# Kernel optimization log

Measured on AMD Instinct MI355X. Metric: run time of the kernel, lower is better.

## Reference

```python
import jax, jax.numpy as jnp
import numpy as np

B, S, D, H, DFF = 4, 1024, 1024, 16, 4096
MAX_LEN = 1024
DK = D // H
EPS = 1e-5


def _ln(x, g, b):
    m = jnp.mean(x, axis=-1, keepdims=True)
    v = jnp.mean(jnp.square(x - m), axis=-1, keepdims=True)
    return (x - m) / jnp.sqrt(v + EPS) * g + b


def setup_inputs() -> dict:
    key = jax.random.key(0)
    ks = jax.random.split(key, 16)
    s = 0.02
    inp = {
        "x": jax.random.normal(ks[0], (B, S, D), jnp.float32),
        "wq": jax.random.normal(ks[1], (D, D), jnp.float32) * s,
        "bq": jnp.zeros((D,), jnp.float32),
        "wk": jax.random.normal(ks[2], (D, D), jnp.float32) * s,
        "bk": jnp.zeros((D,), jnp.float32),
        "wv": jax.random.normal(ks[3], (D, D), jnp.float32) * s,
        "bv": jnp.zeros((D,), jnp.float32),
        "wo": jax.random.normal(ks[4], (D, D), jnp.float32) * s,
        "bo": jnp.zeros((D,), jnp.float32),
        "rel_table": jax.random.normal(ks[5], (2 * MAX_LEN - 1, H), jnp.float32) * s,
        "ln1_g": jnp.ones((D,), jnp.float32),
        "ln1_b": jnp.zeros((D,), jnp.float32),
        "w1": jax.random.normal(ks[6], (D, DFF), jnp.float32) * s,
        "b1": jnp.zeros((DFF,), jnp.float32),
        "w2": jax.random.normal(ks[7], (DFF, D), jnp.float32) * s,
        "b2": jnp.zeros((D,), jnp.float32),
        "ln2_g": jnp.ones((D,), jnp.float32),
        "ln2_b": jnp.zeros((D,), jnp.float32),
        "mask": jnp.ones((B, 1, 1, S), jnp.int32),
    }
    return inp


def reference(x, wq, bq, wk, bk, wv, bv, wo, bo, rel_table,
              ln1_g, ln1_b, w1, b1, w2, b2, ln2_g, ln2_b, mask):
    # --- multi-head attention with relative position bias (post-LN encoder layer, eval mode) ---
    q = (x @ wq + bq).reshape(B, S, H, DK).transpose(0, 2, 1, 3)  # [B,H,S,dk]
    k = (x @ wk + bk).reshape(B, S, H, DK).transpose(0, 2, 1, 3)
    v = (x @ wv + bv).reshape(B, S, H, DK).transpose(0, 2, 1, 3)

    scores = jnp.einsum('bhqd,bhkd->bhqk', q, k) / jnp.sqrt(jnp.float32(DK))

    # relative position bias: table[(q - k + max_len - 1).clip] -> [1,H,S,S]
    coords = jnp.arange(S)[:, None] - jnp.arange(S)[None, :] + (MAX_LEN - 1)
    coords = jnp.clip(coords, 0, 2 * MAX_LEN - 2)
    bias = rel_table[coords]              # [S,S,H]
    scores = scores + bias.transpose(2, 0, 1)[None]

    scores = jnp.where(mask == 0, jnp.float32(-1e9), scores)
    attn = jax.nn.softmax(scores, axis=-1)
    ctx = jnp.einsum('bhqk,bhkd->bhqd', attn, v)
    ctx = ctx.transpose(0, 2, 1, 3).reshape(B, S, D)
    attn_out = ctx @ wo + bo

    x1 = _ln(x + attn_out, ln1_g, ln1_b)

    ff = jax.nn.relu(x1 @ w1 + b1) @ w2 + b2
    return _ln(x1 + ff, ln2_g, ln2_b)
```

## Files before the change

kernel.cpp:

```cpp
#include <hip/hip_runtime.h>
#include <hip/hip_bf16.h>

typedef __hip_bfloat16 bf16;
typedef __attribute__((ext_vector_type(8))) short short8;
typedef __attribute__((ext_vector_type(4))) float f32x4;

#define LOG2E 1.4426950408889634f

typedef const __attribute__((address_space(1))) void* gptr_t;
typedef __attribute__((address_space(3))) void* sptr_t;

__device__ __forceinline__ void async16(void* lds, const void* g) {
  __builtin_amdgcn_global_load_lds((gptr_t)g, (sptr_t)lds, 16, 0, 0);
}

__device__ __forceinline__ float bf2f(unsigned short u) {
  union { unsigned int i; float f; } c; c.i = ((unsigned int)u) << 16; return c.f;
}


__global__ __launch_bounds__(256) void prep_all(
    const float* __restrict__ x, const float* __restrict__ bq,
    const float* __restrict__ bk, const float* __restrict__ bv,
    const float* __restrict__ wq, const float* __restrict__ wk,
    const float* __restrict__ wv, const float* __restrict__ wo,
    const float* __restrict__ w1, const float* __restrict__ w2,
    bf16* __restrict__ xb, float* __restrict__ bqkv,
    bf16* __restrict__ dqkv, bf16* __restrict__ dwo,
    bf16* __restrict__ dw1, bf16* __restrict__ dw2) {
  const int bid = blockIdx.x;
  if (bid < 4096) {
    int i = (bid * 256 + threadIdx.x) * 4;
    float4 v = *(const float4*)(x + i);
    bf16 h4[4] = {__float2bfloat16(v.x), __float2bfloat16(v.y),
                  __float2bfloat16(v.z), __float2bfloat16(v.w)};
    *(uint2*)((unsigned short*)xb + i) = *(uint2*)h4;
    return;
  }
  if (bid == 16384) {
#pragma unroll
    for (int j = 0; j < 12; ++j) {
      int i = j * 256 + threadIdx.x;
      bqkv[i] = (i < 1024) ? bq[i] : (i < 2048 ? bk[i - 1024] : bv[i - 2048]);
    }
    return;
  }
  __shared__ float tl[32][33];
  const int tid = bid - 4096;
  const float* s;
  bf16* d;
  int NN, KK, n0, k0;
  if (tid < 4096) {
    int m = tid >> 10, tile = tid & 1023;
    s = m == 0 ? wq : m == 1 ? wk : m == 2 ? wv : wo;
    d = m < 3 ? dqkv + (size_t)m * 1024 * 1024 : dwo;
    NN = 1024; KK = 1024;
    n0 = (tile & 31) * 32; k0 = (tile >> 5) * 32;
  } else if (tid < 8192) {
    int tile = tid - 4096;
    s = w1; d = dw1; NN = 4096; KK = 1024;
    n0 = (tile & 127) * 32; k0 = (tile >> 7) * 32;
  } else {
    int tile = tid - 8192;
    s = w2; d = dw2; NN = 1024; KK = 4096;
    n0 = (tile & 31) * 32; k0 = (tile >> 5) * 32;
  }
  const int tx = threadIdx.x & 31, ty = threadIdx.x >> 5;
#pragma unroll
  for (int j = 0; j < 4; ++j)
    tl[ty + j * 8][tx] = s[(size_t)(k0 + ty + j * 8) * NN + n0 + tx];
  __syncthreads();
#pragma unroll
  for (int j = 0; j < 4; ++j)
    d[(size_t)(n0 + ty + j * 8) * KK + k0 + tx] =
        __float2bfloat16(tl[tx][ty + j * 8]);
}


template <int RELU, int VT>
__global__ __launch_bounds__(256, 4) void gemm_bt(
    const bf16* __restrict__ A, const bf16* __restrict__ Bt,
    const float* __restrict__ bias, bf16* __restrict__ C,
    bf16* __restrict__ vt, int M, int N, int K) {
  __shared__ bf16 As[2][128 * 32];
  __shared__ bf16 Bs[2][128 * 32];
  const int t = threadIdx.x;
  const int w = t >> 6, l = t & 63;
  const int m0 = blockIdx.x * 128, n0 = blockIdx.y * 128;
  const int wr = (w >> 1) * 64, wc = (w & 1) * 64;
  const int srow = l >> 2, schunk = l & 3;
  const int lm = l & 15, lq = l >> 4;

  f32x4 acc[4][4];
#pragma unroll
  for (int i = 0; i < 4; ++i)
#pragma unroll
    for (int j = 0; j < 4; ++j) acc[i][j] = (f32x4){0.f, 0.f, 0.f, 0.f};

  auto stage = [&](int k0, int d) {
#pragma unroll
    for (int p = 0; p < 2; ++p) {
      int rbase = p * 64 + w * 16;
      int row = rbase + srow;
      int gc = schunk ^ ((row >> 1) & 3);
      async16(&As[d][rbase * 32], A + (size_t)(m0 + row) * K + k0 + gc * 8);
      async16(&Bs[d][rbase * 32], Bt + (size_t)(n0 + row) * K + k0 + gc * 8);
    }
  };

  stage(0, 0);
  const int niter = K >> 5;
  for (int it = 0; it < niter; ++it) {
    const int d = it & 1;
    __syncthreads();
    short8 af[4], bfr[4];
#pragma unroll
    for (int mi = 0; mi < 4; ++mi) {
      int rowa = wr + mi * 16 + lm;
      af[mi] = *(const short8*)&As[d][rowa * 32 + ((lq ^ ((rowa >> 1) & 3)) << 3)];
      int rowb = wc + mi * 16 + lm;
      bfr[mi] = *(const short8*)&Bs[d][rowb * 32 + ((lq ^ ((rowb >> 1) & 3)) << 3)];
    }
    if (it + 1 < niter) stage((it + 1) << 5, d ^ 1);
#pragma unroll
    for (int mi = 0; mi < 4; ++mi)
#pragma unroll
      for (int ni = 0; ni < 4; ++ni)
        acc[mi][ni] = __builtin_amdgcn_mfma_f32_16x16x32_bf16(
            af[mi], bfr[ni], acc[mi][ni], 0, 0, 0);
  }

#pragma unroll
  for (int mi = 0; mi < 4; ++mi)
#pragma unroll
    for (int ni = 0; ni < 4; ++ni) {
      int col = n0 + wc + ni * 16 + lm;
      int row0 = m0 + wr + mi * 16 + lq * 4;
      float bv = bias[col];
      float v[4];
#pragma unroll
      for (int r = 0; r < 4; ++r) {
        v[r] = acc[mi][ni][r] + bv;
        if (RELU) v[r] = fmaxf(v[r], 0.f);
        C[(size_t)(row0 + r) * N + col] = __float2bfloat16(v[r]);
      }
      if (VT && col >= 2048) {
        int vcol = col - 2048;
        int bh = (row0 >> 10) * 16 + (vcol >> 6);
        int dk = vcol & 63;
        int s = row0 & 1023;
        bf16 h4[4] = {__float2bfloat16(v[0]), __float2bfloat16(v[1]),
                      __float2bfloat16(v[2]), __float2bfloat16(v[3])};
        *(uint2*)&vt[((size_t)bh * 64 + dk) * 1024 + s] = *(uint2*)h4;
      }
    }
}

__global__ __launch_bounds__(256, 4) void gemm_bt_splitk(
    const bf16* __restrict__ A, const bf16* __restrict__ Bt,
    bf16* __restrict__ P, int M, int N, int lda, int KS) {
  __shared__ bf16 As[2][128 * 32];
  __shared__ bf16 Bs[2][128 * 32];
  const int t = threadIdx.x;
  const int w = t >> 6, l = t & 63;
  const int m0 = blockIdx.x * 128, n0 = blockIdx.y * 128;
  const int kstart = blockIdx.z * KS;
  const int wr = (w >> 1) * 64, wc = (w & 1) * 64;
  const int srow = l >> 2, schunk = l & 3;
  const int lm = l & 15, lq = l >> 4;

  f32x4 acc[4][4];
#pragma unroll
  for (int i = 0; i < 4; ++i)
#pragma unroll
    for (int j = 0; j < 4; ++j) acc[i][j] = (f32x4){0.f, 0.f, 0.f, 0.f};

  auto stage = [&](int k0, int d) {
#pragma unroll
    for (int p = 0; p < 2; ++p) {
      int rbase = p * 64 + w * 16;
      int row = rbase + srow;
      int gc = schunk ^ ((row >> 1) & 3);
      async16(&As[d][rbase * 32], A + (size_t)(m0 + row) * lda + k0 + gc * 8);
      async16(&Bs[d][rbase * 32], Bt + (size_t)(n0 + row) * lda + k0 + gc * 8);
    }
  };

  stage(kstart, 0);
  const int niter = KS >> 5;
  for (int it = 0; it < niter; ++it) {
    const int d = it & 1;
    __syncthreads();
    short8 af[4], bfr[4];
#pragma unroll
    for (int mi = 0; mi < 4; ++mi) {
      int rowa = wr + mi * 16 + lm;
      af[mi] = *(const short8*)&As[d][rowa * 32 + ((lq ^ ((rowa >> 1) & 3)) << 3)];
      int rowb = wc + mi * 16 + lm;
      bfr[mi] = *(const short8*)&Bs[d][rowb * 32 + ((lq ^ ((rowb >> 1) & 3)) << 3)];
    }
    if (it + 1 < niter) stage(kstart + ((it + 1) << 5), d ^ 1);
#pragma unroll
    for (int mi = 0; mi < 4; ++mi)
#pragma unroll
      for (int ni = 0; ni < 4; ++ni)
        acc[mi][ni] = __builtin_amdgcn_mfma_f32_16x16x32_bf16(
            af[mi], bfr[ni], acc[mi][ni], 0, 0, 0);
  }
  bf16* Pz = P + (size_t)blockIdx.z * M * N;
#pragma unroll
  for (int mi = 0; mi < 4; ++mi)
#pragma unroll
    for (int r = 0; r < 4; ++r) {
      int row = m0 + wr + mi * 16 + lq * 4 + r;
#pragma unroll
      for (int ni = 0; ni < 4; ++ni) {
        int col = n0 + wc + ni * 16 + lm;
        Pz[(size_t)row * N + col] = __float2bfloat16(acc[mi][ni][r]);
      }
    }
}


__global__ __launch_bounds__(512, 4) void flash_attn(
    const bf16* __restrict__ qkv, const bf16* __restrict__ vt,
    const float* __restrict__ rel, const int* __restrict__ mask,
    bf16* __restrict__ ctx) {
  __shared__ bf16 Kl[2][64 * 64];
  __shared__ bf16 Vl[2][64 * 64];
  __shared__ bf16 Pl[128 * 64];
  __shared__ float bias_s[2][192];
  __shared__ float mask_s[2][64];

  const int t = threadIdx.x;
  const int w = t >> 6, l = t & 63;
  const int lm = l & 15, lq = l >> 4;
  const int qt = blockIdx.x, bh = blockIdx.y;
  const int b = bh >> 4, h = bh & 15;
  const int q0 = qt * 128;
  const int srow = l >> 3;
  const int gc = (l & 7) ^ srow;
  const int qq = w * 16 + lm;

  auto stage = [&](int d, int k0n) {
    async16(&Kl[d][w * 8 * 64],
            qkv + (size_t)(b * 1024 + k0n + w * 8 + srow) * 3072 + 1024 + h * 64 + gc * 8);
    async16(&Vl[d][w * 8 * 64],
            vt + ((size_t)bh * 64 + w * 8 + srow) * 1024 + k0n + gc * 8);
    if (t < 191) bias_s[d][t] = rel[(q0 - k0n + 960 + t) * 16 + h] * LOG2E;
    if (t < 64) mask_s[d][t] = (mask[b * 1024 + k0n + t] == 0) ? -1.44e9f : 0.f;
  };

#pragma unroll
  for (int p = 0; p < 2; ++p)
    async16(&Pl[(p * 64 + w * 8) * 64],
            qkv + (size_t)(b * 1024 + q0 + p * 64 + w * 8 + srow) * 3072 + h * 64 + gc * 8);
  stage(0, 0);
  __syncthreads();

  short8 qf[2];
#pragma unroll
  for (int kk = 0; kk < 2; ++kk)
    qf[kk] = *(const short8*)&Pl[qq * 64 + (((kk * 4 + lq) ^ (lm & 7)) << 3)];
  __syncthreads();

  float l_acc = 0.f;
  f32x4 acc_o[4];
#pragma unroll
  for (int j = 0; j < 4; ++j) acc_o[j] = (f32x4){0.f, 0.f, 0.f, 0.f};

  const float C0 = 0.125f * LOG2E;

  for (int kt = 0; kt < 16; ++kt) {
    const int d = kt & 1;
    if (kt < 15) stage(d ^ 1, (kt + 1) * 64);

    f32x4 sa[4];
#pragma unroll
    for (int i = 0; i < 4; ++i) sa[i] = (f32x4){0.f, 0.f, 0.f, 0.f};
#pragma unroll
    for (int kk = 0; kk < 2; ++kk) {
      short8 ak[4];
#pragma unroll
      for (int mi = 0; mi < 4; ++mi) {
        int row = mi * 16 + lm;
        ak[mi] = *(const short8*)&Kl[d][row * 64 + (((kk * 4 + lq) ^ (lm & 7)) << 3)];
      }
#pragma unroll
      for (int mi = 0; mi < 4; ++mi)
        sa[mi] = __builtin_amdgcn_mfma_f32_16x16x32_bf16(ak[mi], qf[kk], sa[mi], 0, 0, 0);
    }

    float m4[4][4];
#pragma unroll
    for (int mi = 0; mi < 4; ++mi)
      *(float4*)m4[mi] = *(const float4*)&mask_s[d][mi * 16 + lq * 4];
#pragma unroll
    for (int mi = 0; mi < 4; ++mi)
#pragma unroll
      for (int r = 0; r < 4; ++r) {
        int kl = mi * 16 + lq * 4 + r;
        float p = __builtin_amdgcn_exp2f(
            fmaf(sa[mi][r], C0, bias_s[d][qq - kl + 63] + m4[mi][r]));
        sa[mi][r] = p;
        l_acc += p;
      }

#pragma unroll
    for (int mi = 0; mi < 4; ++mi) {
      bf16 h4[4];
#pragma unroll
      for (int r = 0; r < 4; ++r) h4[r] = __float2bfloat16(sa[mi][r]);
      int chunk = mi * 2 + (lq >> 1);
      *(uint2*)&Pl[qq * 64 + ((chunk ^ (lm & 7)) << 3) + ((lq & 1) << 2)] =
          *(uint2*)h4;
    }

#pragma unroll
    for (int kk2 = 0; kk2 < 2; ++kk2) {
      short8 pf = *(const short8*)&Pl[qq * 64 + (((kk2 * 4 + lq) ^ (lm & 7)) << 3)];
      short8 vf[4];
#pragma unroll
      for (int ni = 0; ni < 4; ++ni) {
        int rowv = ni * 16 + lm;
        vf[ni] = *(const short8*)&Vl[d][rowv * 64 + (((kk2 * 4 + lq) ^ (lm & 7)) << 3)];
      }
#pragma unroll
      for (int ni = 0; ni < 4; ++ni)
        acc_o[ni] = __builtin_amdgcn_mfma_f32_16x16x32_bf16(pf, vf[ni], acc_o[ni], 0, 0, 0);
    }
    __syncthreads();
  }

  l_acc += __shfl_xor(l_acc, 16);
  l_acc += __shfl_xor(l_acc, 32);
  float linv = 1.f / l_acc;
#pragma unroll
  for (int r = 0; r < 4; ++r) {
    float il = __shfl(linv, lq * 4 + r);
    int qx = w * 16 + lq * 4 + r;
    size_t rowbase = (size_t)(b * 1024 + q0 + qx) * 1024 + h * 64;
#pragma unroll
    for (int ni = 0; ni < 4; ++ni)
      ctx[rowbase + ni * 16 + lm] = __float2bfloat16(acc_o[ni][r] * il);
  }
}


template <int NS>
__global__ __launch_bounds__(256) void ln_resid(
    const float* __restrict__ xin, const bf16* __restrict__ part,
    const float* __restrict__ bias,
    const float* __restrict__ gw, const float* __restrict__ bw,
    float* __restrict__ outf, bf16* __restrict__ outb) {
  const int row = blockIdx.x, t = threadIdx.x;
  const size_t base = (size_t)row * 1024 + t * 4;
  float4 xv = *(const float4*)(xin + base);
  float4 bi = *(const float4*)(bias + t * 4);
  float v0 = xv.x + bi.x, v1 = xv.y + bi.y, v2 = xv.z + bi.z, v3 = xv.w + bi.w;
#pragma unroll
  for (int s = 0; s < NS; ++s) {
    const bf16* p = part + (size_t)s * 4194304 + base;
    ushort4 pv = *(const ushort4*)p;
    v0 += bf2f(pv.x); v1 += bf2f(pv.y); v2 += bf2f(pv.z); v3 += bf2f(pv.w);
  }
  float s1 = v0 + v1 + v2 + v3;
  float s2 = v0 * v0 + v1 * v1 + v2 * v2 + v3 * v3;
#pragma unroll
  for (int o = 1; o < 64; o <<= 1) {
    s1 += __shfl_xor(s1, o);
    s2 += __shfl_xor(s2, o);
  }
  __shared__ float red[8];
  const int w = t >> 6, l = t & 63;
  if (l == 0) { red[w] = s1; red[4 + w] = s2; }
  __syncthreads();
  float S1 = red[0] + red[1] + red[2] + red[3];
  float S2 = red[4] + red[5] + red[6] + red[7];
  float mean = S1 * (1.f / 1024.f);
  float var = S2 * (1.f / 1024.f) - mean * mean;
  float rstd = rsqrtf(var + 1e-5f);
  float4 gv = *(const float4*)(gw + t * 4);
  float4 bv = *(const float4*)(bw + t * 4);
  float o0 = (v0 - mean) * rstd * gv.x + bv.x;
  float o1 = (v1 - mean) * rstd * gv.y + bv.y;
  float o2 = (v2 - mean) * rstd * gv.z + bv.z;
  float o3 = (v3 - mean) * rstd * gv.w + bv.w;
  if (outf) {
    float4 ov = {o0, o1, o2, o3};
    *(float4*)(outf + base) = ov;
  }
  if (outb) {
    bf16 h4[4] = {__float2bfloat16(o0), __float2bfloat16(o1),
                  __float2bfloat16(o2), __float2bfloat16(o3)};
    *(uint2*)((unsigned short*)outb + base) = *(uint2*)h4;
  }
}


extern "C" void kernel_launch(void* const* d_in, const int* in_sizes, int n_in,
                              void* d_out, int out_size, void* d_ws, size_t ws_size,
                              hipStream_t stream) {
  (void)in_sizes; (void)n_in; (void)out_size; (void)ws_size;
  const float* x   = (const float*)d_in[0];
  const float* wq  = (const float*)d_in[1];
  const float* bq  = (const float*)d_in[2];
  const float* wk  = (const float*)d_in[3];
  const float* bk  = (const float*)d_in[4];
  const float* wv  = (const float*)d_in[5];
  const float* bv  = (const float*)d_in[6];
  const float* wo  = (const float*)d_in[7];
  const float* bo  = (const float*)d_in[8];
  const float* rel = (const float*)d_in[9];
  const float* g1  = (const float*)d_in[10];
  const float* be1 = (const float*)d_in[11];
  const float* w1  = (const float*)d_in[12];
  const float* b1  = (const float*)d_in[13];
  const float* w2  = (const float*)d_in[14];
  const float* b2  = (const float*)d_in[15];
  const float* g2  = (const float*)d_in[16];
  const float* be2 = (const float*)d_in[17];
  const int* mask  = (const int*)d_in[18];
  float* out = (float*)d_out;

  char* ws = (char*)d_ws;
  bf16*  xb      = (bf16*)(ws + 0);
  bf16*  wqkv_t  = (bf16*)(ws + 8388608);
  bf16*  wo_t    = (bf16*)(ws + 14680064);
  bf16*  w1_t    = (bf16*)(ws + 16777216);
  bf16*  ctx_b   = (bf16*)(ws + 25165824);
  bf16*  x1b     = (bf16*)(ws + 33554432);
  bf16*  qkv_b   = (bf16*)(ws + 41943040);
  bf16*  vtb     = (bf16*)(ws + 67108864);
  bf16*  part_wo = (bf16*)(ws + 41943040);
  bf16*  h1      = (bf16*)(ws + 41943040);
  bf16*  part_ff = (bf16*)(ws + 0);
  bf16*  w2_t    = (bf16*)(ws + 75497472);
  float* x1f     = (float*)(ws + 83886080);
  float* bqkv    = (float*)(ws + 100663296);

  prep_all<<<16385, 256, 0, stream>>>(x, bq, bk, bv, wq, wk, wv, wo, w1, w2,
                                      xb, bqkv, wqkv_t, wo_t, w1_t, w2_t);

  gemm_bt<0, 1><<<dim3(32, 24), 256, 0, stream>>>(
      xb, wqkv_t, bqkv, qkv_b, vtb, 4096, 3072, 1024);
  flash_attn<<<dim3(8, 64), 512, 0, stream>>>(qkv_b, vtb, rel, mask, ctx_b);
  gemm_bt_splitk<<<dim3(32, 8, 4), 256, 0, stream>>>(
      ctx_b, wo_t, part_wo, 4096, 1024, 1024, 256);
  ln_resid<4><<<4096, 256, 0, stream>>>(x, part_wo, bo, g1, be1, x1f, x1b);
  gemm_bt<1, 0><<<dim3(32, 32), 256, 0, stream>>>(
      x1b, w1_t, b1, h1, nullptr, 4096, 4096, 1024);
  gemm_bt_splitk<<<dim3(32, 8, 4), 256, 0, stream>>>(
      h1, w2_t, part_ff, 4096, 1024, 4096, 1024);
  ln_resid<4><<<4096, 256, 0, stream>>>(x1f, part_ff, b2, g2, be2, out, nullptr);
}
```

Measured before the change: 326.9 us.

## Double GEMM K-tile to 64 and halve split-K factor for output projections

Both bf16 GEMM kernels now stage 64-wide K slices (128x64 tiles, 8-chunk XOR swizzle) instead of 32, halving the number of barrier/prefetch iterations and issuing two MFMA k-steps per sync. LDS per block doubles to 64 KB and the occupancy hint of 4 blocks is dropped. The Wo and W2 split-K launches go from 4 to 2 partitions, which halves the partial-sum traffic read by the layernorm kernels but gives each block a longer K loop and launches fewer blocks.

```diff
diff --git a/kernel.cpp b/kernel.cpp
--- a/kernel.cpp
+++ b/kernel.cpp
@@ -78,17 +78,17 @@
 
 
 template <int RELU, int VT>
-__global__ __launch_bounds__(256, 4) void gemm_bt(
+__global__ __launch_bounds__(256) void gemm_bt(
     const bf16* __restrict__ A, const bf16* __restrict__ Bt,
     const float* __restrict__ bias, bf16* __restrict__ C,
     bf16* __restrict__ vt, int M, int N, int K) {
-  __shared__ bf16 As[2][128 * 32];
-  __shared__ bf16 Bs[2][128 * 32];
+  __shared__ bf16 As[2][128 * 64];
+  __shared__ bf16 Bs[2][128 * 64];
   const int t = threadIdx.x;
   const int w = t >> 6, l = t & 63;
   const int m0 = blockIdx.x * 128, n0 = blockIdx.y * 128;
   const int wr = (w >> 1) * 64, wc = (w & 1) * 64;
-  const int srow = l >> 2, schunk = l & 3;
+  const int srow = l >> 3, scol = l & 7;
   const int lm = l & 15, lq = l >> 4;
 
   f32x4 acc[4][4];
@@ -99,35 +99,38 @@
 
   auto stage = [&](int k0, int d) {
 #pragma unroll
-    for (int p = 0; p < 2; ++p) {
-      int rbase = p * 64 + w * 16;
-      int row = rbase + srow;
-      int gc = schunk ^ ((row >> 1) & 3);
-      async16(&As[d][rbase * 32], A + (size_t)(m0 + row) * K + k0 + gc * 8);
-      async16(&Bs[d][rbase * 32], Bt + (size_t)(n0 + row) * K + k0 + gc * 8);
+    for (int p = 0; p < 4; ++p) {
+      int row = p * 32 + w * 8 + srow;
+      int gc = scol ^ (row & 7);
+      async16(&As[d][(p * 32 + w * 8) * 64], A + (size_t)(m0 + row) * K + k0 + gc * 8);
+      async16(&Bs[d][(p * 32 + w * 8) * 64], Bt + (size_t)(n0 + row) * K + k0 + gc * 8);
     }
   };
 
   stage(0, 0);
-  const int niter = K >> 5;
+  const int niter = K >> 6;
   for (int it = 0; it < niter; ++it) {
     const int d = it & 1;
     __syncthreads();
-    short8 af[4], bfr[4];
-#pragma unroll
-    for (int mi = 0; mi < 4; ++mi) {
-      int rowa = wr + mi * 16 + lm;
-      af[mi] = *(const short8*)&As[d][rowa * 32 + ((lq ^ ((rowa >> 1) & 3)) << 3)];
-      int rowb = wc + mi * 16 + lm;
-      bfr[mi] = *(const short8*)&Bs[d][rowb * 32 + ((lq ^ ((rowb >> 1) & 3)) << 3)];
-    }
-    if (it + 1 < niter) stage((it + 1) << 5, d ^ 1);
-#pragma unroll
-    for (int mi = 0; mi < 4; ++mi)
-#pragma unroll
-      for (int ni = 0; ni < 4; ++ni)
-        acc[mi][ni] = __builtin_amdgcn_mfma_f32_16x16x32_bf16(
-            af[mi], bfr[ni], acc[mi][ni], 0, 0, 0);
+    short8 af[2][4], bfr[2][4];
+#pragma unroll
+    for (int kk = 0; kk < 2; ++kk)
+#pragma unroll
+      for (int mi = 0; mi < 4; ++mi) {
+        int rowa = wr + mi * 16 + lm;
+        af[kk][mi] = *(const short8*)&As[d][rowa * 64 + (((kk * 4 + lq) ^ (rowa & 7)) << 3)];
+        int rowb = wc + mi * 16 + lm;
+        bfr[kk][mi] = *(const short8*)&Bs[d][rowb * 64 + (((kk * 4 + lq) ^ (rowb & 7)) << 3)];
+      }
+    if (it + 1 < niter) stage((it + 1) << 6, d ^ 1);
+#pragma unroll
+    for (int kk = 0; kk < 2; ++kk)
+#pragma unroll
+      for (int mi = 0; mi < 4; ++mi)
+#pragma unroll
+        for (int ni = 0; ni < 4; ++ni)
+          acc[mi][ni] = __builtin_amdgcn_mfma_f32_16x16x32_bf16(
+              af[kk][mi], bfr[kk][ni], acc[mi][ni], 0, 0, 0);
   }
 
 #pragma unroll
@@ -156,17 +159,17 @@
     }
 }
 
-__global__ __launch_bounds__(256, 4) void gemm_bt_splitk(
+__global__ __launch_bounds__(256) void gemm_bt_splitk(
     const bf16* __restrict__ A, const bf16* __restrict__ Bt,
     bf16* __restrict__ P, int M, int N, int lda, int KS) {
-  __shared__ bf16 As[2][128 * 32];
-  __shared__ bf16 Bs[2][128 * 32];
+  __shared__ bf16 As[2][128 * 64];
+  __shared__ bf16 Bs[2][128 * 64];
   const int t = threadIdx.x;
   const int w = t >> 6, l = t & 63;
   const int m0 = blockIdx.x * 128, n0 = blockIdx.y * 128;
   const int kstart = blockIdx.z * KS;
   const int wr = (w >> 1) * 64, wc = (w & 1) * 64;
-  const int srow = l >> 2, schunk = l & 3;
+  const int srow = l >> 3, scol = l & 7;
   const int lm = l & 15, lq = l >> 4;
 
   f32x4 acc[4][4];
@@ -177,35 +180,38 @@
 
   auto stage = [&](int k0, int d) {
 #pragma unroll
-    for (int p = 0; p < 2; ++p) {
-      int rbase = p * 64 + w * 16;
-      int row = rbase + srow;
-      int gc = schunk ^ ((row >> 1) & 3);
-      async16(&As[d][rbase * 32], A + (size_t)(m0 + row) * lda + k0 + gc * 8);
-      async16(&Bs[d][rbase * 32], Bt + (size_t)(n0 + row) * lda + k0 + gc * 8);
+    for (int p = 0; p < 4; ++p) {
+      int row = p * 32 + w * 8 + srow;
+      int gc = scol ^ (row & 7);
+      async16(&As[d][(p * 32 + w * 8) * 64], A + (size_t)(m0 + row) * lda + k0 + gc * 8);
+      async16(&Bs[d][(p * 32 + w * 8) * 64], Bt + (size_t)(n0 + row) * lda + k0 + gc * 8);
     }
   };
 
   stage(kstart, 0);
-  const int niter = KS >> 5;
+  const int niter = KS >> 6;
   for (int it = 0; it < niter; ++it) {
     const int d = it & 1;
     __syncthreads();
-    short8 af[4], bfr[4];
-#pragma unroll
-    for (int mi = 0; mi < 4; ++mi) {
-      int rowa = wr + mi * 16 + lm;
-      af[mi] = *(const short8*)&As[d][rowa * 32 + ((lq ^ ((rowa >> 1) & 3)) << 3)];
-      int rowb = wc + mi * 16 + lm;
-      bfr[mi] = *(const short8*)&Bs[d][rowb * 32 + ((lq ^ ((rowb >> 1) & 3)) << 3)];
-    }
-    if (it + 1 < niter) stage(kstart + ((it + 1) << 5), d ^ 1);
-#pragma unroll
-    for (int mi = 0; mi < 4; ++mi)
-#pragma unroll
-      for (int ni = 0; ni < 4; ++ni)
-        acc[mi][ni] = __builtin_amdgcn_mfma_f32_16x16x32_bf16(
-            af[mi], bfr[ni], acc[mi][ni], 0, 0, 0);
+    short8 af[2][4], bfr[2][4];
+#pragma unroll
+    for (int kk = 0; kk < 2; ++kk)
+#pragma unroll
+      for (int mi = 0; mi < 4; ++mi) {
+        int rowa = wr + mi * 16 + lm;
+        af[kk][mi] = *(const short8*)&As[d][rowa * 64 + (((kk * 4 + lq) ^ (rowa & 7)) << 3)];
+        int rowb = wc + mi * 16 + lm;
+        bfr[kk][mi] = *(const short8*)&Bs[d][rowb * 64 + (((kk * 4 + lq) ^ (rowb & 7)) << 3)];
+      }
+    if (it + 1 < niter) stage(kstart + ((it + 1) << 6), d ^ 1);
+#pragma unroll
+    for (int kk = 0; kk < 2; ++kk)
+#pragma unroll
+      for (int mi = 0; mi < 4; ++mi)
+#pragma unroll
+        for (int ni = 0; ni < 4; ++ni)
+          acc[mi][ni] = __builtin_amdgcn_mfma_f32_16x16x32_bf16(
+              af[kk][mi], bfr[kk][ni], acc[mi][ni], 0, 0, 0);
   }
   bf16* Pz = P + (size_t)blockIdx.z * M * N;
 #pragma unroll
@@ -445,12 +451,12 @@
   gemm_bt<0, 1><<<dim3(32, 24), 256, 0, stream>>>(
       xb, wqkv_t, bqkv, qkv_b, vtb, 4096, 3072, 1024);
   flash_attn<<<dim3(8, 64), 512, 0, stream>>>(qkv_b, vtb, rel, mask, ctx_b);
-  gemm_bt_splitk<<<dim3(32, 8, 4), 256, 0, stream>>>(
-      ctx_b, wo_t, part_wo, 4096, 1024, 1024, 256);
-  ln_resid<4><<<4096, 256, 0, stream>>>(x, part_wo, bo, g1, be1, x1f, x1b);
+  gemm_bt_splitk<<<dim3(32, 8, 2), 256, 0, stream>>>(
+      ctx_b, wo_t, part_wo, 4096, 1024, 1024, 512);
+  ln_resid<2><<<4096, 256, 0, stream>>>(x, part_wo, bo, g1, be1, x1f, x1b);
   gemm_bt<1, 0><<<dim3(32, 32), 256, 0, stream>>>(
       x1b, w1_t, b1, h1, nullptr, 4096, 4096, 1024);
-  gemm_bt_splitk<<<dim3(32, 8, 4), 256, 0, stream>>>(
-      h1, w2_t, part_ff, 4096, 1024, 4096, 1024);
-  ln_resid<4><<<4096, 256, 0, stream>>>(x1f, part_ff, b2, g2, be2, out, nullptr);
-}
+  gemm_bt_splitk<<<dim3(32, 8, 2), 256, 0, stream>>>(
+      h1, w2_t, part_ff, 4096, 1024, 4096, 2048);
+  ln_resid<2><<<4096, 256, 0, stream>>>(x1f, part_ff, b2, g2, be2, out, nullptr);
+}
```

Measured after the change: 323.2 us. No clear change (-1.1%).
